# Performance work log

Hardware: AMD Instinct MI355X
Metric: run time of the kernel (lower is better)

## Reference

```python
import jax, jax.numpy as jnp
import numpy as np

M = 41
RHO = 4.0
HDIM = 10
NMODES = 2
BATCH = 16384


def triplet_index(m_size, rho):
    # reduced PBC triplet index set: n >= m, |m|,|n|,|m+n| <= (M-1)/2, |m*n| <= rho*(M-1)/2
    h = (m_size - 1) // 2
    idx = [(m, n) for m in range(-h, h + 1) for n in range(m, h + 1)
           if abs(m + n) <= h and abs(m * n) <= rho * h]
    return np.array(idx, dtype=np.int32)

IDX = triplet_index(M, RHO)
S = len(IDX)


def _c(a):
    # last-dim-2 real tensor -> complex
    return jax.lax.complex(a[..., 0], a[..., 1])


def setup_inputs() -> dict:
    key = jax.random.key(0)
    ks = jax.random.split(key, 6)
    x = jax.random.normal(ks[0], (BATCH, M, NMODES, 2), dtype=jnp.float32)
    task_info = jax.random.uniform(ks[1], (BATCH, 4), dtype=jnp.float32)  # col 0 = power in dBm
    pbc_C = 0.01 * jax.random.normal(ks[2], (S, 2), dtype=jnp.float32)  # complex PBC coeffs
    W1 = jax.random.normal(ks[3], (HDIM, NMODES, S, 2), dtype=jnp.float32) / np.sqrt(2.0 * NMODES * S)
    b1 = jnp.zeros((HDIM, 2), dtype=jnp.float32)
    W2 = jax.random.normal(ks[4], (HDIM, NMODES, M, 2), dtype=jnp.float32) / np.sqrt(2.0 * NMODES * M)
    b2 = jnp.zeros((HDIM, 2), dtype=jnp.float32)
    m_idx = jnp.asarray(IDX[:, 0], dtype=jnp.int32)
    n_idx = jnp.asarray(IDX[:, 1], dtype=jnp.int32)
    return {"x": x, "task_info": task_info, "pbc_C": pbc_C,
            "W1": W1, "b1": b1, "W2": W2, "b2": b2,
            "m_idx": m_idx, "n_idx": n_idx}


def _nonlinear_features(E, m_idx, n_idx):
    # E: [B, M, 2] complex -> [B, 2, S]; Manakov dual-pol triplets:
    # F[p] = (E[c+m,p]*conj(E[c+m+n,p]) + E[c+m,q]*conj(E[c+m+n,q])) * E[c+n,p]
    c = E.shape[1] // 2
    A = E[:, c + m_idx, :] * jnp.conj(E[:, c + m_idx + n_idx, :])  # [B, S, 2]
    F = (A + A[..., ::-1]) * E[:, c + n_idx, :]                    # [B, S, 2]
    return jnp.transpose(F, (0, 2, 1))                             # [B, 2, S]


def _conv_full(Wc, bc, inp):
    # ComplexConv1d whose kernel spans the whole input length (output length 1) -> [B, out]
    return jnp.einsum('oik,bik->bo', Wc, inp) + bc


def _forward(x, task_info, pbc_C, W1, b1, W2, b2, m_idx, n_idx):
    E = _c(x)                                    # [B, M, 2] complex64
    c = M // 2
    P = 10.0 ** (task_info[:, 0] / 10.0) / NMODES  # [B] launch power per mode
    F = _nonlinear_features(E, m_idx, n_idx)     # [B, 2, S]
    # EqAMPBC: center symbol + P * (triplet features . complex coeffs)
    pbc_out = E[:, c, :] + P[:, None] * jnp.einsum('bps,s->bp', F, _c(pbc_C))  # [B, 2]
    w1, bb1, w2, bb2 = _c(W1), _c(b1), _c(W2), _c(b2)
    # A = cat([f1(fo), f1(fo with pols flipped)], dim=-1) -> [B, hdim, 2]
    A = jnp.stack([_conv_full(w1, bb1, F), _conv_full(w1, bb1, F[:, ::-1, :])], axis=-1)
    Et = jnp.transpose(E, (0, 2, 1))             # [B, 2, M]
    Bm = jnp.stack([_conv_full(w2, bb2, Et), _conv_full(w2, bb2, Et[:, ::-1, :])], axis=-1)
    term = jnp.sum(A * Bm * jnp.conj(Bm) + jnp.conj(A) * Bm * Bm, axis=1)  # [B, 2]
    out = pbc_out + (1e-4 / np.sqrt(HDIM)) * term * (P[:, None] ** 2)
    return jnp.stack([out.real, out.imag], axis=-1)  # [B, 2, 2] float32


def reference(x, task_info, pbc_C, W1, b1, W2, b2, m_idx, n_idx):
    return _forward(x, task_info, pbc_C, W1, b1, W2, b2, m_idx, n_idx)
```

## Files before the change

kernel.cpp:

```cpp
#include <hip/hip_runtime.h>
#include <hip/hip_bf16.h>

typedef short bf16x8 __attribute__((ext_vector_type(8)));
typedef float f32x16 __attribute__((ext_vector_type(16)));

#define NCOL  32
#define KS1   112
#define KS2   12
#define ESTR  264

#define WP_OFF   0
#define W2P_OFF  344064

#define MET_OFF  10824
#define SUM_OFF  14544
#define SUM2_OFF 39120
#define LDS_BYTES 63696

__device__ __forceinline__ unsigned short f2bf(float f) {
    union { float f; unsigned u; } v; v.f = f;
    unsigned r = v.u + 0x7FFFu + ((v.u >> 16) & 1u);
    return (unsigned short)(r >> 16);
}
__device__ __forceinline__ float bfl(unsigned u) {
    union { unsigned q; float f; } v; v.q = u << 16; return v.f;
}
__device__ __forceinline__ float bfh(unsigned u) {
    union { unsigned q; float f; } v; v.q = u & 0xffff0000u; return v.f;
}
__device__ __forceinline__ unsigned pk2(float a, float b) {
    __hip_bfloat162 h = __float22bfloat162_rn(make_float2(a, b));
    unsigned u; __builtin_memcpy(&u, &h, 4); return u;
}
__device__ __forceinline__ bf16x8 asbf(uint4 v) {
    union { uint4 u; bf16x8 b; } z; z.u = v; return z.b;
}
__device__ __forceinline__ f32x16 zero16() {
    f32x16 z;
#pragma unroll
    for (int i = 0; i < 16; ++i) z[i] = 0.f;
    return z;
}

__global__ void prep_kernel(const float* __restrict__ W1,
                            const float* __restrict__ W2,
                            const float* __restrict__ pbcC,
                            unsigned short* __restrict__ Wp,
                            unsigned short* __restrict__ W2p, int S) {
    int idx = blockIdx.x * 256 + threadIdx.x;
    const int N1 = KS1 * 3 * 64 * 2;
    const int N2 = KS2 * 3 * 64 * 2;
    if (idx < N1) {
        int ks = idx / 384, rem = idx - ks * 384;
        int mt = rem >> 7; rem &= 127;
        int lane = rem >> 1, jh = rem & 1;
        int row = mt * 32 + (lane & 31);
        int kg  = ks * 16 + (lane >> 5) * 8 + jh * 4;
        int s   = kg >> 2;
        float2 wj0 = make_float2(0.f, 0.f), wj1 = make_float2(0.f, 0.f);
        int p = 0, r = 0;
        if (s < S) {
            if (row < 80) {
                int o = row >> 2; p = (row >> 1) & 1; r = row & 1;
                wj0 = ((const float2*)W1)[(size_t)(o * 2 + 0) * S + s];
                wj1 = ((const float2*)W1)[(size_t)(o * 2 + 1) * S + s];
            } else if (row < 84) {
                p = (row >> 1) & 1; r = row & 1;
                wj0 = ((const float2*)pbcC)[s];
            }
        }
        ushort4 h; unsigned short us[4];
#pragma unroll
        for (int t = 0; t < 4; ++t) {
            int i = t & 1, cc = t >> 1, j2 = i ^ p;
            float2 w = j2 ? wj1 : wj0;
            float v = (cc == 0) ? (r ? w.y : w.x) : (r ? w.x : -w.y);
            us[t] = f2bf(v);
        }
        h.x = us[0]; h.y = us[1]; h.z = us[2]; h.w = us[3];
        ((ushort4*)Wp)[idx] = h;
        return;
    }
    idx -= N1;
    if (idx < N2) {
        int ks = idx / 384, rem = idx - ks * 384;
        int mt = rem >> 7; rem &= 127;
        int lane = rem >> 1, jh = rem & 1;
        int row = mt * 32 + (lane & 31);
        int kg  = ks * 16 + (lane >> 5) * 8 + jh * 4;
        int m   = kg >> 2;
        float2 wj0 = make_float2(0.f, 0.f), wj1 = make_float2(0.f, 0.f);
        int p = 0, r = 0;
        if (m < 41 && row < 80) {
            int o = row >> 2; p = (row >> 1) & 1; r = row & 1;
            wj0 = ((const float2*)W2)[(o * 2 + 0) * 41 + m];
            wj1 = ((const float2*)W2)[(o * 2 + 1) * 41 + m];
        }
        ushort4 h; unsigned short us[4];
#pragma unroll
        for (int t = 0; t < 4; ++t) {
            int i = t & 1, cc = t >> 1, j2 = i ^ p;
            float2 w = j2 ? wj1 : wj0;
            float v = (cc == 0) ? (r ? w.y : w.x) : (r ? w.x : -w.y);
            us[t] = f2bf(v);
        }
        h.x = us[0]; h.y = us[1]; h.z = us[2]; h.w = us[3];
        ((ushort4*)W2p)[idx] = h;
    }
}

__global__ __launch_bounds__(512, 4) void eqsonn_kernel(
    const float* __restrict__ x, const float* __restrict__ task,
    const unsigned short* __restrict__ Wp,
    const unsigned short* __restrict__ W2p,
    const int* __restrict__ m_idx, const int* __restrict__ n_idx,
    const float* __restrict__ b1, const float* __restrict__ b2,
    float* __restrict__ out, int B, int S)
{
    __shared__ alignas(16) char ldsb[LDS_BYTES];
    const int tid  = threadIdx.x;
    const int lane = tid & 63;
    const int w    = __builtin_amdgcn_readfirstlane(tid >> 6);
    const int col  = lane & 31;
    const int kha  = lane >> 5;
    const int b0   = blockIdx.x * NCOL;

    for (int e = tid; e < 41 * NCOL; e += 512) {
        int bb = e / 41, k = e - bb * 41;
        int bs = b0 + bb; if (bs > B - 1) bs = B - 1;
        float4 v = ((const float4*)x)[(size_t)bs * 41 + k];
        ushort4 h;
        h.x = f2bf(v.x); h.y = f2bf(v.y); h.z = f2bf(v.z); h.w = f2bf(v.w);
        *(ushort4*)(ldsb + k * ESTR + bb * 8) = h;
    }
    if (tid < 464) {
        int m = 0, n = 0;
        if (tid < S) { m = m_idx[tid]; n = n_idx[tid]; }
        unsigned offM = (unsigned)((20 + m) * ESTR);
        unsigned offB = (unsigned)((20 + m + n) * ESTR);
        unsigned offN = (unsigned)((20 + n) * ESTR);
        *(uint2*)(ldsb + MET_OFF + tid * 8) = make_uint2(offM | (offB << 16), offN);
    }
    __syncthreads();

    const char* Ebase = ldsb + col * 8;
    auto ldM4 = [&](int ks) -> uint4 {
        return *(const uint4*)(ldsb + MET_OFF + (ks * 4 + kha * 2) * 8);
    };
    auto ldE = [&](unsigned off) -> uint2 {
        return *(const uint2*)(Ebase + off);
    };
    auto fbuild = [&](uint2 em, uint2 eq, uint2 en, unsigned& lo, unsigned& hi) {
        float m0r = bfl(em.x), m0i = bfh(em.x), m1r = bfl(em.y), m1i = bfh(em.y);
        float q0r = bfl(eq.x), q0i = bfh(eq.x), q1r = bfl(eq.y), q1i = bfh(eq.y);
        float n0r = bfl(en.x), n0i = bfh(en.x), n1r = bfl(en.y), n1i = bfh(en.y);
        float sr = m0r * q0r + m0i * q0i + m1r * q1r + m1i * q1i;
        float si = m0i * q0r - m0r * q0i + m1i * q1r - m1r * q1i;
        float F0r = sr * n0r - si * n0i, F0i = sr * n0i + si * n0r;
        float F1r = sr * n1r - si * n1i, F1i = sr * n1i + si * n1r;
        lo = pk2(F0r, F1r); hi = pk2(F0i, F1i);
    };

    f32x16 ac0 = zero16(), ac1 = zero16(), ac2 = zero16();
    {
        const int ks0 = w * 14;
        const short* Wp16 = (const short*)Wp;
        uint4 M = ldM4(ks0);
        uint2 e0 = ldE(M.x & 0xffffu), e1 = ldE(M.x >> 16), e2 = ldE(M.y);
        uint2 e3 = ldE(M.z & 0xffffu), e4 = ldE(M.z >> 16), e5 = ldE(M.w);
        uint4 Mc = ldM4(ks0 + 1);
        const short* ap0 = Wp16 + (size_t)ks0 * 1536 + lane * 8;
        bf16x8 A0 = *(const bf16x8*)(ap0);
        bf16x8 A1 = *(const bf16x8*)(ap0 + 512);
        bf16x8 A2 = *(const bf16x8*)(ap0 + 1024);
        for (int ks = ks0; ks < ks0 + 14; ++ks) {
            int ksn = (ks + 1 < KS1) ? ks + 1 : KS1 - 1;
            const short* apn = Wp16 + (size_t)ksn * 1536 + lane * 8;
            bf16x8 N0 = *(const bf16x8*)(apn);
            bf16x8 N1 = *(const bf16x8*)(apn + 512);
            bf16x8 N2 = *(const bf16x8*)(apn + 1024);
            uint2 f0 = ldE(Mc.x & 0xffffu), f1v = ldE(Mc.x >> 16), f2v = ldE(Mc.y);
            uint2 f3 = ldE(Mc.z & 0xffffu), f4v = ldE(Mc.z >> 16), f5v = ldE(Mc.w);
            uint4 Mn = ldM4(ks + 2);
            unsigned g0, g1, g2, g3;
            fbuild(e0, e1, e2, g0, g1);
            fbuild(e3, e4, e5, g2, g3);
            bf16x8 bfr = asbf(make_uint4(g0, g1, g2, g3));
            ac0 = __builtin_amdgcn_mfma_f32_32x32x16_bf16(A0, bfr, ac0, 0, 0, 0);
            ac1 = __builtin_amdgcn_mfma_f32_32x32x16_bf16(A1, bfr, ac1, 0, 0, 0);
            ac2 = __builtin_amdgcn_mfma_f32_32x32x16_bf16(A2, bfr, ac2, 0, 0, 0);
            e0 = f0; e1 = f1v; e2 = f2v; e3 = f3; e4 = f4v; e5 = f5v; Mc = Mn;
            A0 = N0; A1 = N1; A2 = N2;
        }
    }

    __syncthreads();
    float* Reg = (float*)(ldsb + ((w < 4) ? SUM_OFF : SUM2_OFF));
    const int ph = w & 3;
    auto dump = [&](f32x16 a, int baserow, bool add) {
#pragma unroll
        for (int reg = 0; reg < 16; ++reg) {
            int row = baserow + (reg & 3) + 8 * (reg >> 2) + 4 * kha;
            int idx = row * 32 + col;
            if (add) Reg[idx] += a[reg]; else Reg[idx] = a[reg];
        }
    };
    for (int p = 0; p < 4; ++p) {
        if (ph == p) {
            bool add = (p != 0);
            dump(ac0, 0, add); dump(ac1, 32, add); dump(ac2, 64, add);
        }
        __syncthreads();
    }

    f32x16 bc0 = zero16(), bc1 = zero16(), bc2 = zero16();
    {
        const short* W216 = (const short*)W2p;
        for (int ks2 = w; ks2 < KS2; ks2 += 8) {
            const short* ap = W216 + (size_t)ks2 * 1536 + lane * 8;
            bf16x8 A0 = *(const bf16x8*)(ap);
            bf16x8 A1 = *(const bf16x8*)(ap + 512);
            bf16x8 A2 = *(const bf16x8*)(ap + 1024);
            unsigned g[4];
#pragma unroll
            for (int j = 0; j < 2; ++j) {
                int m = ks2 * 4 + kha * 2 + j;
                int mc = m < 41 ? m : 40;
                uint2 ue = *(const uint2*)(ldsb + mc * ESTR + col * 8);
                unsigned lo = (ue.x & 0xffffu) | (ue.y << 16);
                unsigned hi = (ue.x >> 16) | (ue.y & 0xffff0000u);
                if (m >= 41) { lo = 0u; hi = 0u; }
                g[j * 2] = lo; g[j * 2 + 1] = hi;
            }
            bf16x8 bfr = asbf(make_uint4(g[0], g[1], g[2], g[3]));
            bc0 = __builtin_amdgcn_mfma_f32_32x32x16_bf16(A0, bfr, bc0, 0, 0, 0);
            bc1 = __builtin_amdgcn_mfma_f32_32x32x16_bf16(A1, bfr, bc1, 0, 0, 0);
            bc2 = __builtin_amdgcn_mfma_f32_32x32x16_bf16(A2, bfr, bc2, 0, 0, 0);
        }
    }
    __syncthreads();
    for (int p = 0; p < 4; ++p) {
        if (ph == p) {
            bool add = (p != 0);
            dump(bc0, 96, add); dump(bc1, 128, add); dump(bc2, 160, add);
        }
        __syncthreads();
    }

    {
        float4* S1 = (float4*)(ldsb + SUM_OFF);
        float4* S2 = (float4*)(ldsb + SUM2_OFF);
#pragma unroll
        for (int i = 0; i < 3; ++i) {
            int idx = tid + i * 512;
            float4 a = S1[idx], b = S2[idx];
            a.x += b.x; a.y += b.y; a.z += b.z; a.w += b.w;
            S1[idx] = a;
        }
    }
    __syncthreads();

    if (w == 0 && lane < NCOL) {
        const float* Sum = (const float*)(ldsb + SUM_OFF);
        int c = lane;
        float pr0 = Sum[80 * 32 + c], pi0 = Sum[81 * 32 + c];
        float pr1 = Sum[82 * 32 + c], pi1 = Sum[83 * 32 + c];
        float t0 = 0.f, t1 = 0.f, t2 = 0.f, t3 = 0.f;
#pragma unroll
        for (int o = 0; o < 10; ++o) {
            float b2r = b2[o * 2], b2i = b2[o * 2 + 1];
            float b1r = b1[o * 2], b1i = b1[o * 2 + 1];
            int rb = o * 4;
            float B0r = Sum[(96 + rb + 0) * 32 + c] + b2r;
            float B0i = Sum[(96 + rb + 1) * 32 + c] + b2i;
            float B1r = Sum[(96 + rb + 2) * 32 + c] + b2r;
            float B1i = Sum[(96 + rb + 3) * 32 + c] + b2i;
            float A0r = Sum[(rb + 0) * 32 + c] + b1r;
            float A0i = Sum[(rb + 1) * 32 + c] + b1i;
            float A1r = Sum[(rb + 2) * 32 + c] + b1r;
            float A1i = Sum[(rb + 3) * 32 + c] + b1i;
            float g0 = 2.f * (A0r * B0r + A0i * B0i);
            t0 += g0 * B0r; t1 += g0 * B0i;
            float g1 = 2.f * (A1r * B1r + A1i * B1i);
            t2 += g1 * B1r; t3 += g1 * B1i;
        }
        int b = b0 + c;
        if (b < B) {
            float dbm = task[(size_t)b * 4];
            float P   = exp2f(dbm * 0.33219280948873623f) * 0.5f;
            float kP2 = 3.1622776601683794e-05f * P * P;
            float4 Ec = ((const float4*)x)[(size_t)b * 41 + 20];
            float4 o4;
            o4.x = Ec.x + P * pr0 + kP2 * t0;
            o4.y = Ec.y + P * pi0 + kP2 * t1;
            o4.z = Ec.z + P * pr1 + kP2 * t2;
            o4.w = Ec.w + P * pi1 + kP2 * t3;
            ((float4*)out)[b] = o4;
        }
    }
}

extern "C" void kernel_launch(void* const* d_in, const int* in_sizes, int n_in,
                              void* d_out, int out_size, void* d_ws, size_t ws_size,
                              hipStream_t stream) {
    const float* x     = (const float*)d_in[0];
    const float* task  = (const float*)d_in[1];
    const float* pbcC  = (const float*)d_in[2];
    const float* W1    = (const float*)d_in[3];
    const float* b1    = (const float*)d_in[4];
    const float* W2    = (const float*)d_in[5];
    const float* b2    = (const float*)d_in[6];
    const int*   m_idx = (const int*)d_in[7];
    const int*   n_idx = (const int*)d_in[8];
    float* out = (float*)d_out;

    int S = in_sizes[7];
    int B = in_sizes[0] / (41 * 2 * 2);

    char* ws = (char*)d_ws;
    unsigned short* Wp  = (unsigned short*)(ws + WP_OFF);
    unsigned short* W2p = (unsigned short*)(ws + W2P_OFF);

    int prep_n = KS1 * 3 * 64 * 2 + KS2 * 3 * 64 * 2;
    prep_kernel<<<(prep_n + 255) / 256, 256, 0, stream>>>(W1, W2, pbcC, Wp, W2p, S);

    int grid = (B + NCOL - 1) / NCOL;
    eqsonn_kernel<<<grid, 512, 0, stream>>>(x, task, Wp, W2p, m_idx, n_idx,
                                            b1, b2, out, B, S);
}
```

Baseline: 98.55 us.

## Drop unused MFMA row tile, keep E in fp32 LDS, merge reduction passes

```diff
diff --git a/kernel.cpp b/kernel.cpp
--- a/kernel.cpp
+++ b/kernel.cpp
@@ -3,30 +3,26 @@
 
 typedef short bf16x8 __attribute__((ext_vector_type(8)));
 typedef float f32x16 __attribute__((ext_vector_type(16)));
+typedef float f32x4  __attribute__((ext_vector_type(4)));
+typedef float f32x2  __attribute__((ext_vector_type(2)));
 
 #define NCOL  32
 #define KS1   112
 #define KS2   12
-#define ESTR  264
+#define ESTR  528
 
 #define WP_OFF   0
-#define W2P_OFF  344064
-
-#define MET_OFF  10824
-#define SUM_OFF  14544
-#define SUM2_OFF 39120
-#define LDS_BYTES 63696
+#define W2P_OFF  229376
+
+#define MET_OFF  21648
+#define SUM_OFF  25360
+#define SUM2_OFF 41744
+#define LDS_BYTES 58128
 
 __device__ __forceinline__ unsigned short f2bf(float f) {
     union { float f; unsigned u; } v; v.f = f;
     unsigned r = v.u + 0x7FFFu + ((v.u >> 16) & 1u);
     return (unsigned short)(r >> 16);
-}
-__device__ __forceinline__ float bfl(unsigned u) {
-    union { unsigned q; float f; } v; v.q = u << 16; return v.f;
-}
-__device__ __forceinline__ float bfh(unsigned u) {
-    union { unsigned q; float f; } v; v.q = u & 0xffff0000u; return v.f;
 }
 __device__ __forceinline__ unsigned pk2(float a, float b) {
     __hip_bfloat162 h = __float22bfloat162_rn(make_float2(a, b));
@@ -48,10 +44,10 @@
                             unsigned short* __restrict__ Wp,
                             unsigned short* __restrict__ W2p, int S) {
     int idx = blockIdx.x * 256 + threadIdx.x;
-    const int N1 = KS1 * 3 * 64 * 2;
-    const int N2 = KS2 * 3 * 64 * 2;
+    const int N1 = KS1 * 2 * 64 * 2;
+    const int N2 = KS2 * 2 * 64 * 2;
     if (idx < N1) {
-        int ks = idx / 384, rem = idx - ks * 384;
+        int ks = idx >> 8, rem = idx & 255;
         int mt = rem >> 7; rem &= 127;
         int lane = rem >> 1, jh = rem & 1;
         int row = mt * 32 + (lane & 31);
@@ -60,11 +56,11 @@
         float2 wj0 = make_float2(0.f, 0.f), wj1 = make_float2(0.f, 0.f);
         int p = 0, r = 0;
         if (s < S) {
-            if (row < 80) {
+            if (row < 40) {
                 int o = row >> 2; p = (row >> 1) & 1; r = row & 1;
                 wj0 = ((const float2*)W1)[(size_t)(o * 2 + 0) * S + s];
                 wj1 = ((const float2*)W1)[(size_t)(o * 2 + 1) * S + s];
-            } else if (row < 84) {
+            } else if (row < 44) {
                 p = (row >> 1) & 1; r = row & 1;
                 wj0 = ((const float2*)pbcC)[s];
             }
@@ -83,7 +79,7 @@
     }
     idx -= N1;
     if (idx < N2) {
-        int ks = idx / 384, rem = idx - ks * 384;
+        int ks = idx >> 8, rem = idx & 255;
         int mt = rem >> 7; rem &= 127;
         int lane = rem >> 1, jh = rem & 1;
         int row = mt * 32 + (lane & 31);
@@ -91,7 +87,7 @@
         int m   = kg >> 2;
         float2 wj0 = make_float2(0.f, 0.f), wj1 = make_float2(0.f, 0.f);
         int p = 0, r = 0;
-        if (m < 41 && row < 80) {
+        if (m < 41 && row < 40) {
             int o = row >> 2; p = (row >> 1) & 1; r = row & 1;
             wj0 = ((const float2*)W2)[(o * 2 + 0) * 41 + m];
             wj1 = ((const float2*)W2)[(o * 2 + 1) * 41 + m];
@@ -129,9 +125,8 @@
         int bb = e / 41, k = e - bb * 41;
         int bs = b0 + bb; if (bs > B - 1) bs = B - 1;
         float4 v = ((const float4*)x)[(size_t)bs * 41 + k];
-        ushort4 h;
-        h.x = f2bf(v.x); h.y = f2bf(v.y); h.z = f2bf(v.z); h.w = f2bf(v.w);
-        *(ushort4*)(ldsb + k * ESTR + bb * 8) = h;
+        f32x4 pv; pv.x = v.x; pv.y = v.z; pv.z = v.y; pv.w = v.w;
+        *(f32x4*)(ldsb + k * ESTR + bb * 16) = pv;
     }
     if (tid < 464) {
         int m = 0, n = 0;
@@ -143,44 +138,43 @@
     }
     __syncthreads();
 
-    const char* Ebase = ldsb + col * 8;
+    const char* Ebase = ldsb + col * 16;
     auto ldM4 = [&](int ks) -> uint4 {
         return *(const uint4*)(ldsb + MET_OFF + (ks * 4 + kha * 2) * 8);
     };
-    auto ldE = [&](unsigned off) -> uint2 {
-        return *(const uint2*)(Ebase + off);
+    auto ldE = [&](unsigned off) -> f32x4 {
+        return *(const f32x4*)(Ebase + off);
     };
-    auto fbuild = [&](uint2 em, uint2 eq, uint2 en, unsigned& lo, unsigned& hi) {
-        float m0r = bfl(em.x), m0i = bfh(em.x), m1r = bfl(em.y), m1i = bfh(em.y);
-        float q0r = bfl(eq.x), q0i = bfh(eq.x), q1r = bfl(eq.y), q1i = bfh(eq.y);
-        float n0r = bfl(en.x), n0i = bfh(en.x), n1r = bfl(en.y), n1i = bfh(en.y);
-        float sr = m0r * q0r + m0i * q0i + m1r * q1r + m1i * q1i;
-        float si = m0i * q0r - m0r * q0i + m1i * q1r - m1r * q1i;
-        float F0r = sr * n0r - si * n0i, F0i = sr * n0i + si * n0r;
-        float F1r = sr * n1r - si * n1i, F1i = sr * n1i + si * n1r;
-        lo = pk2(F0r, F1r); hi = pk2(F0i, F1i);
+    auto fbuild = [&](f32x4 em, f32x4 eq, f32x4 en, unsigned& lo, unsigned& hi) {
+        f32x2 mr = em.xy, mi = em.zw;
+        f32x2 qr = eq.xy, qi = eq.zw;
+        f32x2 nr = en.xy, ni = en.zw;
+        f32x2 t = mr * qr + mi * qi;
+        f32x2 u = mi * qr - mr * qi;
+        float sr = t.x + t.y, si = u.x + u.y;
+        f32x2 Fr = sr * nr - si * ni;
+        f32x2 Fi = sr * ni + si * nr;
+        lo = pk2(Fr.x, Fr.y); hi = pk2(Fi.x, Fi.y);
     };
 
-    f32x16 ac0 = zero16(), ac1 = zero16(), ac2 = zero16();
+    f32x16 ac0 = zero16(), ac1 = zero16();
     {
         const int ks0 = w * 14;
         const short* Wp16 = (const short*)Wp;
         uint4 M = ldM4(ks0);
-        uint2 e0 = ldE(M.x & 0xffffu), e1 = ldE(M.x >> 16), e2 = ldE(M.y);
-        uint2 e3 = ldE(M.z & 0xffffu), e4 = ldE(M.z >> 16), e5 = ldE(M.w);
+        f32x4 e0 = ldE(M.x & 0xffffu), e1 = ldE(M.x >> 16), e2 = ldE(M.y);
+        f32x4 e3 = ldE(M.z & 0xffffu), e4 = ldE(M.z >> 16), e5 = ldE(M.w);
         uint4 Mc = ldM4(ks0 + 1);
-        const short* ap0 = Wp16 + (size_t)ks0 * 1536 + lane * 8;
+        const short* ap0 = Wp16 + (size_t)ks0 * 1024 + lane * 8;
         bf16x8 A0 = *(const bf16x8*)(ap0);
         bf16x8 A1 = *(const bf16x8*)(ap0 + 512);
-        bf16x8 A2 = *(const bf16x8*)(ap0 + 1024);
         for (int ks = ks0; ks < ks0 + 14; ++ks) {
             int ksn = (ks + 1 < KS1) ? ks + 1 : KS1 - 1;
-            const short* apn = Wp16 + (size_t)ksn * 1536 + lane * 8;
+            const short* apn = Wp16 + (size_t)ksn * 1024 + lane * 8;
             bf16x8 N0 = *(const bf16x8*)(apn);
             bf16x8 N1 = *(const bf16x8*)(apn + 512);
-            bf16x8 N2 = *(const bf16x8*)(apn + 1024);
-            uint2 f0 = ldE(Mc.x & 0xffffu), f1v = ldE(Mc.x >> 16), f2v = ldE(Mc.y);
-            uint2 f3 = ldE(Mc.z & 0xffffu), f4v = ldE(Mc.z >> 16), f5v = ldE(Mc.w);
+            f32x4 f0 = ldE(Mc.x & 0xffffu), f1v = ldE(Mc.x >> 16), f2v = ldE(Mc.y);
+            f32x4 f3 = ldE(Mc.z & 0xffffu), f4v = ldE(Mc.z >> 16), f5v = ldE(Mc.w);
             uint4 Mn = ldM4(ks + 2);
             unsigned g0, g1, g2, g3;
             fbuild(e0, e1, e2, g0, g1);
@@ -188,61 +182,50 @@
             bf16x8 bfr = asbf(make_uint4(g0, g1, g2, g3));
             ac0 = __builtin_amdgcn_mfma_f32_32x32x16_bf16(A0, bfr, ac0, 0, 0, 0);
             ac1 = __builtin_amdgcn_mfma_f32_32x32x16_bf16(A1, bfr, ac1, 0, 0, 0);
-            ac2 = __builtin_amdgcn_mfma_f32_32x32x16_bf16(A2, bfr, ac2, 0, 0, 0);
             e0 = f0; e1 = f1v; e2 = f2v; e3 = f3; e4 = f4v; e5 = f5v; Mc = Mn;
-            A0 = N0; A1 = N1; A2 = N2;
-        }
-    }
-
-    __syncthreads();
-    float* Reg = (float*)(ldsb + ((w < 4) ? SUM_OFF : SUM2_OFF));
-    const int ph = w & 3;
-    auto dump = [&](f32x16 a, int baserow, bool add) {
-#pragma unroll
-        for (int reg = 0; reg < 16; ++reg) {
-            int row = baserow + (reg & 3) + 8 * (reg >> 2) + 4 * kha;
-            int idx = row * 32 + col;
-            if (add) Reg[idx] += a[reg]; else Reg[idx] = a[reg];
-        }
-    };
-    for (int p = 0; p < 4; ++p) {
-        if (ph == p) {
-            bool add = (p != 0);
-            dump(ac0, 0, add); dump(ac1, 32, add); dump(ac2, 64, add);
-        }
-        __syncthreads();
-    }
-
-    f32x16 bc0 = zero16(), bc1 = zero16(), bc2 = zero16();
+            A0 = N0; A1 = N1;
+        }
+    }
+
+    f32x16 bc0 = zero16(), bc1 = zero16();
     {
         const short* W216 = (const short*)W2p;
         for (int ks2 = w; ks2 < KS2; ks2 += 8) {
-            const short* ap = W216 + (size_t)ks2 * 1536 + lane * 8;
+            const short* ap = W216 + (size_t)ks2 * 1024 + lane * 8;
             bf16x8 A0 = *(const bf16x8*)(ap);
             bf16x8 A1 = *(const bf16x8*)(ap + 512);
-            bf16x8 A2 = *(const bf16x8*)(ap + 1024);
             unsigned g[4];
 #pragma unroll
             for (int j = 0; j < 2; ++j) {
                 int m = ks2 * 4 + kha * 2 + j;
                 int mc = m < 41 ? m : 40;
-                uint2 ue = *(const uint2*)(ldsb + mc * ESTR + col * 8);
-                unsigned lo = (ue.x & 0xffffu) | (ue.y << 16);
-                unsigned hi = (ue.x >> 16) | (ue.y & 0xffff0000u);
+                f32x4 v = *(const f32x4*)(ldsb + mc * ESTR + col * 16);
+                unsigned lo = pk2(v.x, v.y);
+                unsigned hi = pk2(v.z, v.w);
                 if (m >= 41) { lo = 0u; hi = 0u; }
                 g[j * 2] = lo; g[j * 2 + 1] = hi;
             }
             bf16x8 bfr = asbf(make_uint4(g[0], g[1], g[2], g[3]));
             bc0 = __builtin_amdgcn_mfma_f32_32x32x16_bf16(A0, bfr, bc0, 0, 0, 0);
             bc1 = __builtin_amdgcn_mfma_f32_32x32x16_bf16(A1, bfr, bc1, 0, 0, 0);
-            bc2 = __builtin_amdgcn_mfma_f32_32x32x16_bf16(A2, bfr, bc2, 0, 0, 0);
-        }
-    }
-    __syncthreads();
+        }
+    }
+
+    float* Reg = (float*)(ldsb + ((w < 4) ? SUM_OFF : SUM2_OFF));
+    const int ph = w & 3;
+    auto dump = [&](f32x16 a, int baserow, bool add) {
+#pragma unroll
+        for (int reg = 0; reg < 16; ++reg) {
+            int row = baserow + (reg & 3) + 8 * (reg >> 2) + 4 * kha;
+            int idx = row * 32 + col;
+            if (add) Reg[idx] += a[reg]; else Reg[idx] = a[reg];
+        }
+    };
     for (int p = 0; p < 4; ++p) {
         if (ph == p) {
             bool add = (p != 0);
-            dump(bc0, 96, add); dump(bc1, 128, add); dump(bc2, 160, add);
+            dump(ac0, 0, add); dump(ac1, 32, add);
+            dump(bc0, 64, add); dump(bc1, 96, add);
         }
         __syncthreads();
     }
@@ -251,7 +234,7 @@
         float4* S1 = (float4*)(ldsb + SUM_OFF);
         float4* S2 = (float4*)(ldsb + SUM2_OFF);
 #pragma unroll
-        for (int i = 0; i < 3; ++i) {
+        for (int i = 0; i < 2; ++i) {
             int idx = tid + i * 512;
             float4 a = S1[idx], b = S2[idx];
             a.x += b.x; a.y += b.y; a.z += b.z; a.w += b.w;
@@ -263,18 +246,18 @@
     if (w == 0 && lane < NCOL) {
         const float* Sum = (const float*)(ldsb + SUM_OFF);
         int c = lane;
-        float pr0 = Sum[80 * 32 + c], pi0 = Sum[81 * 32 + c];
-        float pr1 = Sum[82 * 32 + c], pi1 = Sum[83 * 32 + c];
+        float pr0 = Sum[40 * 32 + c], pi0 = Sum[41 * 32 + c];
+        float pr1 = Sum[42 * 32 + c], pi1 = Sum[43 * 32 + c];
         float t0 = 0.f, t1 = 0.f, t2 = 0.f, t3 = 0.f;
 #pragma unroll
         for (int o = 0; o < 10; ++o) {
             float b2r = b2[o * 2], b2i = b2[o * 2 + 1];
             float b1r = b1[o * 2], b1i = b1[o * 2 + 1];
             int rb = o * 4;
-            float B0r = Sum[(96 + rb + 0) * 32 + c] + b2r;
-            float B0i = Sum[(96 + rb + 1) * 32 + c] + b2i;
-            float B1r = Sum[(96 + rb + 2) * 32 + c] + b2r;
-            float B1i = Sum[(96 + rb + 3) * 32 + c] + b2i;
+            float B0r = Sum[(64 + rb + 0) * 32 + c] + b2r;
+            float B0i = Sum[(64 + rb + 1) * 32 + c] + b2i;
+            float B1r = Sum[(64 + rb + 2) * 32 + c] + b2r;
+            float B1i = Sum[(64 + rb + 3) * 32 + c] + b2i;
             float A0r = Sum[(rb + 0) * 32 + c] + b1r;
             float A0i = Sum[(rb + 1) * 32 + c] + b1i;
             float A1r = Sum[(rb + 2) * 32 + c] + b1r;
@@ -321,7 +304,7 @@
     unsigned short* Wp  = (unsigned short*)(ws + WP_OFF);
     unsigned short* W2p = (unsigned short*)(ws + W2P_OFF);
 
-    int prep_n = KS1 * 3 * 64 * 2 + KS2 * 3 * 64 * 2;
+    int prep_n = KS1 * 2 * 64 * 2 + KS2 * 2 * 64 * 2;
     prep_kernel<<<(prep_n + 255) / 256, 256, 0, stream>>>(W1, W2, pbcC, Wp, W2p, S);
 
     int grid = (B + NCOL - 1) / NCOL;
```

After: 90.30 us. 8.4% less time.
